# Optimization experiments

Hardware: AMD Instinct MI355X
Metric: run time of the kernel (lower is better)

Reference implementation:

```python
import jax, jax.numpy as jnp
import numpy as np

B, T, W, HP = 1, 64, 88, 48   # batch, frames, pitches, hidden_per_pitch
NU, NH, K = 24, 4, 25          # n_unit, n_heads, neighborhood window
HD = NU // NH                  # head dim = 6
HL = NU // 2                   # LSTM hidden per direction = 12


def _lstm_bidir(x, w_ih, w_hh, b_ih, b_hh):
    # x: [N, T, In]; w_ih: [2, 4*HL, In]; w_hh: [2, 4*HL, HL]; biases: [2, 4*HL]
    N = x.shape[0]
    def run(Wih, Whh, bih, bhh, reverse):
        def step(carry, xt):
            h, c = carry
            g = xt @ Wih.T + h @ Whh.T + bih + bhh
            i, f, gg, o = jnp.split(g, 4, axis=-1)  # torch gate order i,f,g,o
            c = jax.nn.sigmoid(f) * c + jax.nn.sigmoid(i) * jnp.tanh(gg)
            h = jax.nn.sigmoid(o) * jnp.tanh(c)
            return (h, c), h
        init = (jnp.zeros((N, HL), x.dtype), jnp.zeros((N, HL), x.dtype))
        _, ys = jax.lax.scan(step, init, jnp.swapaxes(x, 0, 1), reverse=reverse)
        return jnp.swapaxes(ys, 0, 1)
    return jnp.concatenate([run(w_ih[0], w_hh[0], b_ih[0], b_hh[0], False),
                            run(w_ih[1], w_hh[1], b_ih[1], b_hh[1], True)], axis=-1)


def _natten2d(x, qkv_w, qkv_b, rpb, proj_w, proj_b):
    # Neighborhood attention over 2D grid [B, Hh, Ww] with KxK window clamped at borders.
    Bn, Hh, Ww, C = x.shape
    qkv = (x @ qkv_w.T + qkv_b).reshape(Bn, Hh, Ww, 3, NH, HD)
    q = qkv[..., 0, :, :] * (HD ** -0.5)
    k = qkv[..., 1, :, :]
    v = qkv[..., 2, :, :]
    half = K // 2
    ar = jnp.arange(K)
    idx_i = jnp.clip(jnp.arange(Hh) - half, 0, Hh - K)[:, None] + ar  # [Hh,K]
    idx_j = jnp.clip(jnp.arange(Ww) - half, 0, Ww - K)[:, None] + ar  # [Ww,K]
    kg = k[:, idx_i][:, :, :, idx_j]  # [B,Hh,K,Ww,K,NH,HD]
    vg = v[:, idx_i][:, :, :, idx_j]
    ri = idx_i - jnp.arange(Hh)[:, None] + (K - 1)  # relative pos bias indices [Hh,K]
    rj = idx_j - jnp.arange(Ww)[:, None] + (K - 1)  # [Ww,K]
    bias = rpb[:, ri][:, :, :, rj]                  # [NH,Hh,K,Ww,K]
    logits = jnp.einsum('bijnd,biajcnd->bnijac', q, kg)
    logits = logits + jnp.transpose(bias, (0, 1, 3, 2, 4))[None]
    attn = jax.nn.softmax(logits.reshape(Bn, NH, Hh, Ww, K * K), axis=-1)
    attn = attn.reshape(Bn, NH, Hh, Ww, K, K)
    out = jnp.einsum('bnijac,biajcnd->bijnd', attn, vg).reshape(Bn, Hh, Ww, C)
    return out @ proj_w.T + proj_b


def _forward(features, condition, mask, emb, w_ih_l0, w_hh_l0, b_ih_l0, b_hh_l0,
             w_ih_l1, w_hh_l1, b_ih_l1, b_hh_l1, qkv_w, qkv_b, rpb, proj_w, proj_b,
             out_w, out_b):
    # concat: [B,T,88,HP] + [B,T,88,4] + [B,T,88,1] -> [B,T,88,HP+5]
    cat = jnp.concatenate([jnp.transpose(features, (0, 1, 3, 2)), emb[condition],
                           mask[..., None]], axis=-1)
    x = jnp.transpose(cat, (0, 2, 1, 3)).reshape(B * W, T, HP + 5)  # pitchwise LSTM
    x = _lstm_bidir(x, w_ih_l0, w_hh_l0, b_ih_l0, b_hh_l0)
    x = _lstm_bidir(x, w_ih_l1, w_hh_l1, b_ih_l1, b_hh_l1)
    x = jnp.transpose(x.reshape(B, W, T, NU), (0, 2, 1, 3))  # [B,T,88,NU]
    for _ in range(2):  # n_layers=2; Sequential(*[m]*2) => SHARED weights
        x = _natten2d(x, qkv_w, qkv_b, rpb, proj_w, proj_b)
    return x @ out_w.T + out_b  # [B,T,88,5]


def setup_inputs():
    ks = jax.random.split(jax.random.key(0), 24)
    def unif(k, shape, fan):
        s = 1.0 / np.sqrt(fan)
        return jax.random.uniform(k, shape, jnp.float32, -s, s)
    return {
        'features': jax.random.normal(ks[0], (B, T, HP, W), jnp.float32),
        'condition': jax.random.randint(ks[1], (B, T, W), 0, 5),
        'mask': jax.random.uniform(ks[2], (B, T, W), jnp.float32),
        'emb': jax.random.normal(ks[3], (5, 4), jnp.float32),
        'w_ih_l0': unif(ks[4], (2, 4 * HL, HP + 5), HL),
        'w_hh_l0': unif(ks[5], (2, 4 * HL, HL), HL),
        'b_ih_l0': unif(ks[6], (2, 4 * HL), HL),
        'b_hh_l0': unif(ks[7], (2, 4 * HL), HL),
        'w_ih_l1': unif(ks[8], (2, 4 * HL, 2 * HL), HL),
        'w_hh_l1': unif(ks[9], (2, 4 * HL, HL), HL),
        'b_ih_l1': unif(ks[10], (2, 4 * HL), HL),
        'b_hh_l1': unif(ks[11], (2, 4 * HL), HL),
        'qkv_w': unif(ks[12], (3 * NU, NU), NU),
        'qkv_b': unif(ks[13], (3 * NU,), NU),
        'rpb': jax.random.normal(ks[14], (NH, 2 * K - 1, 2 * K - 1), jnp.float32) * 0.02,
        'proj_w': unif(ks[15], (NU, NU), NU),
        'proj_b': unif(ks[16], (NU,), NU),
        'out_w': unif(ks[17], (5, NU), NU),
        'out_b': unif(ks[18], (5,), NU),
    }


def reference(features, condition, mask, emb, w_ih_l0, w_hh_l0, b_ih_l0, b_hh_l0,
              w_ih_l1, w_hh_l1, b_ih_l1, b_hh_l1, qkv_w, qkv_b, rpb, proj_w, proj_b,
              out_w, out_b):
    return _forward(features, condition, mask, emb, w_ih_l0, w_hh_l0, b_ih_l0, b_hh_l0,
                    w_ih_l1, w_hh_l1, b_ih_l1, b_hh_l1, qkv_w, qkv_b, rpb,
                    proj_w, proj_b, out_w, out_b)
```

## Files before the change

kernel.cpp:

```cpp
#include <hip/hip_runtime.h>
#include <hip/hip_bf16.h>

#define NPIX (64*88)
#define NSEQ 88
#define TT 64
#define F0 53
#define GATES 48

typedef __hip_bfloat16 bf16;

__device__ __forceinline__ float frcp(float x){ return __builtin_amdgcn_rcpf(x); }
__device__ __forceinline__ float blo(unsigned u){ return __uint_as_float(u<<16); }
__device__ __forceinline__ float bhi(unsigned u){ return __uint_as_float(u & 0xffff0000u); }

__device__ __forceinline__ void unpack6(uint4 r, float* f){
  f[0] = __uint_as_float(r.x << 16);
  f[1] = __uint_as_float(r.x & 0xffff0000u);
  f[2] = __uint_as_float(r.y << 16);
  f[3] = __uint_as_float(r.y & 0xffff0000u);
  f[4] = __uint_as_float(r.z << 16);
  f[5] = __uint_as_float(r.z & 0xffff0000u);
}

__global__ __launch_bounds__(1024) void k_core(
    const float* __restrict__ feat, const int* __restrict__ cond,
    const float* __restrict__ mask, const float* __restrict__ emb,
    const float* __restrict__ wih0, const float* __restrict__ whh0,
    const float* __restrict__ bih0, const float* __restrict__ bhh0,
    const float* __restrict__ wih1, const float* __restrict__ whh1,
    const float* __restrict__ bih1, const float* __restrict__ bhh1,
    const float* __restrict__ qkv_w, const float* __restrict__ qkv_b,
    float* __restrict__ q, bf16* __restrict__ kh, bf16* __restrict__ vh){
  int n = (blockIdx.x & 7)*11 + (blockIdx.x >> 3);
  int tid = threadIdx.x;
  int wave = tid >> 6; int lane = tid & 63;
  __shared__ float smem[14816];
  float* gbuf = smem;
  float* sx   = smem + 6144;
  float* sw0  = smem + 6144+3392;
  float* w1   = smem + 6144;
  float* sqkv = smem + 6144+2400;
  float* y0   = smem + 6144+4200;
  float* y1   = smem + 6144+5736;
  float* bsum = smem + 14624;

  for (int idx = tid; idx < 2*GATES*F0; idx += 1024) sw0[idx] = wih0[idx];
  for (int idx = tid; idx < TT*F0; idx += 1024){
    int t = idx / F0, f = idx - t*F0;
    float v;
    if (f < 48)      v = feat[(t*48 + f)*88 + n];
    else if (f < 52) v = emb[cond[t*88+n]*4 + (f-48)];
    else             v = mask[t*88+n];
    sx[idx] = v;
  }
  if (tid < 96)       bsum[tid] = bih0[tid] + bhh0[tid];
  else if (tid < 192) bsum[tid] = bih1[tid-96] + bhh1[tid-96];
  __syncthreads();

  #pragma unroll
  for (int r = 0; r < 6; ++r){
    int row = tid + r*1024;
    int d = row / 3072; int rem = row - d*3072;
    int t = rem / 48; int j = rem - t*48;
    const float* xr = sx + t*F0;
    const float* wr = sw0 + (d*GATES + j)*F0;
    float a0=0.f, a1=0.f, a2=0.f, a3=0.f;
    #pragma unroll
    for (int f=0; f<52; f+=4){
      a0 += xr[f  ]*wr[f  ];
      a1 += xr[f+1]*wr[f+1];
      a2 += xr[f+2]*wr[f+2];
      a3 += xr[f+3]*wr[f+3];
    }
    gbuf[(d*TT + t)*GATES + j] = bsum[d*GATES+j] + xr[52]*wr[52] + ((a0+a1)+(a2+a3));
  }
  __syncthreads();

  if (wave >= 2){
    for (int idx = tid-128; idx < 2*GATES*24; idx += 896){
      int row = idx / 24, f = idx - row*24;
      w1[row*25 + f] = wih1[idx];
    }
    for (int idx = tid-128; idx < 72*24; idx += 896){
      int row = idx / 24, f = idx - row*24;
      sqkv[row*25 + f] = qkv_w[idx];
    }
  } else {
    int d = wave;
    int j = (lane < GATES) ? lane : (lane - GATES);
    int u = j % 12; int grp = j / 12;
    float w[12];
    const float* wb = whh0 + (d*GATES + j)*12;
    #pragma unroll
    for (int m=0;m<12;++m) w[m] = wb[m];
    float negs  = (grp==2) ? -2.f : -1.f;
    float amul  = (grp==2) ?  2.f :  1.f;
    float aadd  = (grp==2) ? -1.f :  0.f;
    const float* gb = gbuf + d*TT*GATES + j;
    float hval = 0.f, cval = 0.f;
    int t0 = d ? (TT-1) : 0;
    float gnext = gb[t0*GATES];
    for (int s=0;s<TT;++s){
      int t = d ? (TT-1-s) : s;
      float gg = gnext;
      int tn = d ? max(TT-2-s,0) : min(s+1,TT-1);
      gnext = gb[tn*GATES];
      float h0=__shfl(hval,0), h1=__shfl(hval,1), h2=__shfl(hval,2);
      float h3=__shfl(hval,3), h4=__shfl(hval,4), h5=__shfl(hval,5);
      float h6=__shfl(hval,6), h7=__shfl(hval,7), h8=__shfl(hval,8);
      float h9=__shfl(hval,9), h10=__shfl(hval,10), h11=__shfl(hval,11);
      float a0 = gg + h0*w[0] + h4*w[4] + h8*w[8];
      float a1 = h1*w[1] + h5*w[5] + h9*w[9];
      float a2 = h2*w[2] + h6*w[6] + h10*w[10];
      float a3 = h3*w[3] + h7*w[7] + h11*w[11];
      float dot = (a0+a1)+(a2+a3);
      float act = amul*frcp(1.f + __expf(negs*dot)) + aadd;
      float ai = __shfl(act, u);
      float af = __shfl(act, u+12);
      float ag = __shfl(act, u+24);
      float ao = __shfl(act, u+36);
      float cn = af*cval + ai*ag;
      float th = 2.f*frcp(1.f + __expf(-2.f*cn)) - 1.f;
      hval = ao*th; cval = cn;
      if (lane < 12) y0[t*24 + d*12 + lane] = hval;
    }
  }
  __syncthreads();

  #pragma unroll
  for (int r = 0; r < 6; ++r){
    int row = tid + r*1024;
    int d = row / 3072; int rem = row - d*3072;
    int t = rem / 48; int j = rem - t*48;
    const float* xr = y0 + t*24;
    const float* wr = w1 + (d*GATES + j)*25;
    float a0=0.f, a1=0.f;
    #pragma unroll
    for (int c=0; c<24; c+=2){ a0 += xr[c]*wr[c]; a1 += xr[c+1]*wr[c+1]; }
    gbuf[(d*TT + t)*GATES + j] = bsum[96 + d*GATES+j] + a0 + a1;
  }
  __syncthreads();

  if (wave < 2){
    int d = wave;
    int j = (lane < GATES) ? lane : (lane - GATES);
    int u = j % 12; int grp = j / 12;
    float w[12];
    const float* wb = whh1 + (d*GATES + j)*12;
    #pragma unroll
    for (int m=0;m<12;++m) w[m] = wb[m];
    float negs  = (grp==2) ? -2.f : -1.f;
    float amul  = (grp==2) ?  2.f :  1.f;
    float aadd  = (grp==2) ? -1.f :  0.f;
    const float* gb = gbuf + d*TT*GATES + j;
    float hval = 0.f, cval = 0.f;
    int t0 = d ? (TT-1) : 0;
    float gnext = gb[t0*GATES];
    for (int s=0;s<TT;++s){
      int t = d ? (TT-1-s) : s;
      float gg = gnext;
      int tn = d ? max(TT-2-s,0) : min(s+1,TT-1);
      gnext = gb[tn*GATES];
      float h0=__shfl(hval,0), h1=__shfl(hval,1), h2=__shfl(hval,2);
      float h3=__shfl(hval,3), h4=__shfl(hval,4), h5=__shfl(hval,5);
      float h6=__shfl(hval,6), h7=__shfl(hval,7), h8=__shfl(hval,8);
      float h9=__shfl(hval,9), h10=__shfl(hval,10), h11=__shfl(hval,11);
      float a0 = gg + h0*w[0] + h4*w[4] + h8*w[8];
      float a1 = h1*w[1] + h5*w[5] + h9*w[9];
      float a2 = h2*w[2] + h6*w[6] + h10*w[10];
      float a3 = h3*w[3] + h7*w[7] + h11*w[11];
      float dot = (a0+a1)+(a2+a3);
      float act = amul*frcp(1.f + __expf(negs*dot)) + aadd;
      float ai = __shfl(act, u);
      float af = __shfl(act, u+12);
      float ag = __shfl(act, u+24);
      float ao = __shfl(act, u+36);
      float cn = af*cval + ai*ag;
      float th = 2.f*frcp(1.f + __expf(-2.f*cn)) - 1.f;
      hval = ao*th; cval = cn;
      if (lane < 12) y1[t*24 + d*12 + lane] = hval;
    }
  }
  __syncthreads();

  for (int idx = tid; idx < TT*72; idx += 1024){
    int gq = idx % 72; int t = idx / 72;
    int p = t*88 + n;
    const float* xr = y1 + t*24;
    const float* wr = sqkv + gq*25;
    float a0=0.f, a1=0.f;
    #pragma unroll
    for (int c=0; c<24; c+=2){ a0 += xr[c]*wr[c]; a1 += xr[c+1]*wr[c+1]; }
    float acc = qkv_b[gq] + a0 + a1;
    int s = gq/24, rem = gq - s*24;
    if (s==0) q[p*24+rem] = acc*0.4082482904638631f;
    else {
      int hh = rem/6, pos = rem - hh*6;
      bf16* dst = (s==1) ? kh : vh;
      dst[((size_t)hh*NPIX + p)*8 + pos] = __float2bfloat16(acc);
    }
  }
}

__global__ __launch_bounds__(256) void k_attn1(
    const float* __restrict__ q, const bf16* __restrict__ kh,
    const bf16* __restrict__ vh, const float* __restrict__ rpb,
    const float* __restrict__ pw, const float* __restrict__ pb,
    const float* __restrict__ qkv_w, const float* __restrict__ qkv_b,
    float* __restrict__ q2, bf16* __restrict__ kh2, bf16* __restrict__ vh2){
  int p = blockIdx.x; int tid = threadIdx.x;
  int h = tid >> 6; int lane = tid & 63;
  int i = p / 88, j = p - i*88;
  int si = min(max(i-12,0),39), sj = min(max(j-12,0),63);
  __shared__ float aorow[24];
  __shared__ float xrow[24];

  float qv[6];
  #pragma unroll
  for (int d=0; d<6; ++d) qv[d] = q[p*24 + h*6 + d];
  const uint4* kb = (const uint4*)(kh + (size_t)h*NPIX*8);
  const uint4* vb = (const uint4*)(vh + (size_t)h*NPIX*8);
  float lgv[10]; int roff[10];
  float lmax = -1e30f;
  #pragma unroll
  for (int it=0; it<10; ++it){
    int nb = lane + it*64;
    bool valid = nb < 625;
    int nbc = valid ? nb : 624;
    int a = nbc/25, cc = nbc - a*25;
    int gi = si + a, gj = sj + cc;
    int row = gi*88+gj;
    roff[it] = row;
    float kr[6];
    unpack6(kb[row], kr);
    float lg = qv[0]*kr[0]+qv[1]*kr[1]+qv[2]*kr[2]+qv[3]*kr[3]+qv[4]*kr[4]+qv[5]*kr[5];
    lg += rpb[(h*49 + (gi - i + 24))*49 + (gj - j + 24)];
    lg = valid ? lg : -1e30f;
    lgv[it] = lg;
    lmax = fmaxf(lmax, lg);
  }
  #pragma unroll
  for (int off=32; off; off>>=1) lmax = fmaxf(lmax, __shfl_xor(lmax, off));
  float lsum = 0.f;
  #pragma unroll
  for (int it=0; it<10; ++it){
    float pe = __expf(lgv[it]-lmax);
    lgv[it] = pe; lsum += pe;
  }
  #pragma unroll
  for (int off=32; off; off>>=1) lsum += __shfl_xor(lsum, off);
  float acc[6] = {0,0,0,0,0,0};
  #pragma unroll
  for (int it=0; it<10; ++it){
    float vr[6];
    unpack6(vb[roff[it]], vr);
    float pe = lgv[it];
    #pragma unroll
    for (int d=0; d<6; ++d) acc[d] += pe*vr[d];
  }
  #pragma unroll
  for (int d=0; d<6; ++d){
    #pragma unroll
    for (int off=32; off; off>>=1) acc[d] += __shfl_xor(acc[d], off);
  }
  if (lane == 0){
    float inv = frcp(lsum);
    #pragma unroll
    for (int d=0; d<6; ++d) aorow[h*6+d] = acc[d]*inv;
  }
  __syncthreads();

  if (tid < 24){
    float a2 = pb[tid];
    const float* wr = pw + tid*24;
    #pragma unroll
    for (int c=0;c<24;++c) a2 += aorow[c]*wr[c];
    xrow[tid] = a2;
  }
  __syncthreads();

  if (tid < 72){
    float a2 = qkv_b[tid];
    const float* wr = qkv_w + tid*24;
    #pragma unroll
    for (int c=0;c<24;++c) a2 += xrow[c]*wr[c];
    int s = tid/24, rem = tid - s*24;
    if (s==0) q2[p*24+rem] = a2*0.4082482904638631f;
    else {
      int hh = rem/6, pos = rem - hh*6;
      bf16* dst = (s==1) ? kh2 : vh2;
      dst[((size_t)hh*NPIX + p)*8 + pos] = __float2bfloat16(a2);
    }
  }
}

__global__ __launch_bounds__(512) void k_attn(
    const float* __restrict__ q, const bf16* __restrict__ kh,
    const bf16* __restrict__ vh, const float* __restrict__ rpb,
    float* __restrict__ ao){
  int b = blockIdx.x;
  int h = b / 704; int rem = b - h*704;
  int ti = rem / 44, tj = rem - ti*44;
  int i0 = ti*4, j0 = tj*2;
  int tid = threadIdx.x;
  int w = tid >> 6; int lane = tid & 63;
  int osi = min(max(i0-12,0),39);
  int osj = min(max(j0-12,0),63);

  __shared__ unsigned kt[728*5];
  __shared__ unsigned vt[728*5];
  const uint4* kg = (const uint4*)(kh + (size_t)h*NPIX*8);
  const uint4* vg = (const uint4*)(vh + (size_t)h*NPIX*8);
  for (int idx = tid; idx < 728; idx += 512){
    int a = idx / 26, cc = idx - a*26;
    int gi = min(osi + a, 63), gj = min(osj + cc, 87);
    int src = gi*88 + gj;
    uint4 kr = kg[src];
    uint4 vr = vg[src];
    int o = idx*5;
    kt[o] = kr.x; kt[o+1] = kr.y; kt[o+2] = kr.z;
    vt[o] = vr.x; vt[o+1] = vr.y; vt[o+2] = vr.z;
  }
  __syncthreads();

  int pi = i0 + (w>>1), pj = j0 + (w&1);
  int p = pi*88 + pj;
  int dsi = min(max(pi-12,0),39) - osi;
  int dsj = min(max(pj-12,0),63) - osj;
  int rbi = osi + dsi - pi + 24;
  int rbj = osj + dsj - pj + 24;

  float qv[6];
  #pragma unroll
  for (int d=0; d<6; ++d) qv[d] = q[p*24 + h*6 + d];

  float lgv[10]; int rof[10];
  float lmax = -1e30f;
  #pragma unroll
  for (int it=0; it<10; ++it){
    int nb = lane + it*64;
    bool valid = nb < 625;
    int nbc = valid ? nb : 624;
    int a = nbc/25, cc = nbc - a*25;
    int r5 = ((a+dsi)*26 + (cc+dsj))*5;
    rof[it] = r5;
    unsigned k0 = kt[r5], k1 = kt[r5+1], k2 = kt[r5+2];
    float lg = qv[0]*blo(k0)+qv[1]*bhi(k0)+qv[2]*blo(k1)
             + qv[3]*bhi(k1)+qv[4]*blo(k2)+qv[5]*bhi(k2);
    lg += rpb[(h*49 + (a + rbi))*49 + (cc + rbj)];
    lg = valid ? lg : -1e30f;
    lgv[it] = lg;
    lmax = fmaxf(lmax, lg);
  }
  #pragma unroll
  for (int off=32; off; off>>=1) lmax = fmaxf(lmax, __shfl_xor(lmax, off));
  float lsum = 0.f;
  #pragma unroll
  for (int it=0; it<10; ++it){
    float pe = __expf(lgv[it]-lmax);
    lgv[it] = pe; lsum += pe;
  }
  #pragma unroll
  for (int off=32; off; off>>=1) lsum += __shfl_xor(lsum, off);
  float acc[6] = {0,0,0,0,0,0};
  #pragma unroll
  for (int it=0; it<10; ++it){
    int r5 = rof[it];
    unsigned v0 = vt[r5], v1 = vt[r5+1], v2 = vt[r5+2];
    float pe = lgv[it];
    acc[0] += pe*blo(v0); acc[1] += pe*bhi(v0);
    acc[2] += pe*blo(v1); acc[3] += pe*bhi(v1);
    acc[4] += pe*blo(v2); acc[5] += pe*bhi(v2);
  }
  #pragma unroll
  for (int d=0; d<6; ++d){
    #pragma unroll
    for (int off=32; off; off>>=1) acc[d] += __shfl_xor(acc[d], off);
  }
  if (lane == 0){
    float inv = frcp(lsum);
    #pragma unroll
    for (int d=0; d<6; ++d) ao[p*24 + h*6 + d] = acc[d]*inv;
  }
}

__global__ __launch_bounds__(64) void k_proj_out(const float* __restrict__ ain,
    const float* __restrict__ pw, const float* __restrict__ pb,
    const float* __restrict__ ow, const float* __restrict__ ob,
    float* __restrict__ out){
  int p = blockIdx.x; int tid = threadIdx.x;
  __shared__ float arow[24];
  __shared__ float xrow[24];
  if (tid < 24) arow[tid] = ain[p*24+tid];
  __syncthreads();
  if (tid < 24){
    float a2 = pb[tid];
    const float* wr = pw + tid*24;
    #pragma unroll
    for (int c=0;c<24;++c) a2 += arow[c]*wr[c];
    xrow[tid] = a2;
  }
  __syncthreads();
  if (tid < 5){
    float a2 = ob[tid];
    const float* wr = ow + tid*24;
    #pragma unroll
    for (int c=0;c<24;++c) a2 += xrow[c]*wr[c];
    out[p*5+tid] = a2;
  }
}

extern "C" void kernel_launch(void* const* d_in, const int* in_sizes, int n_in,
                              void* d_out, int out_size, void* d_ws, size_t ws_size,
                              hipStream_t stream) {
  const float* feat    = (const float*)d_in[0];
  const int*   cond    = (const int*)  d_in[1];
  const float* mask    = (const float*)d_in[2];
  const float* emb     = (const float*)d_in[3];
  const float* w_ih_l0 = (const float*)d_in[4];
  const float* w_hh_l0 = (const float*)d_in[5];
  const float* b_ih_l0 = (const float*)d_in[6];
  const float* b_hh_l0 = (const float*)d_in[7];
  const float* w_ih_l1 = (const float*)d_in[8];
  const float* w_hh_l1 = (const float*)d_in[9];
  const float* b_ih_l1 = (const float*)d_in[10];
  const float* b_hh_l1 = (const float*)d_in[11];
  const float* qkv_w   = (const float*)d_in[12];
  const float* qkv_b   = (const float*)d_in[13];
  const float* rpb     = (const float*)d_in[14];
  const float* proj_w  = (const float*)d_in[15];
  const float* proj_b  = (const float*)d_in[16];
  const float* out_w   = (const float*)d_in[17];
  const float* out_b   = (const float*)d_in[18];
  float* out = (float*)d_out;

  float* ws  = (float*)d_ws;
  float* Q1  = ws;
  float* Q2  = Q1 + 135168;
  float* AO  = Q2 + 135168;
  bf16*  KH1 = (bf16*)(AO + 135168);
  bf16*  VH1 = KH1 + 180224;
  bf16*  KH2 = VH1 + 180224;
  bf16*  VH2 = KH2 + 180224;

  k_core<<<NSEQ, 1024, 0, stream>>>(
      feat, cond, mask, emb,
      w_ih_l0, w_hh_l0, b_ih_l0, b_hh_l0,
      w_ih_l1, w_hh_l1, b_ih_l1, b_hh_l1,
      qkv_w, qkv_b, Q1, KH1, VH1);

  k_attn1<<<NPIX, 256, 0, stream>>>(
      Q1, KH1, VH1, rpb, proj_w, proj_b, qkv_w, qkv_b,
      Q2, KH2, VH2);

  k_attn<<<4*16*44, 512, 0, stream>>>(Q2, KH2, VH2, rpb, AO);

  k_proj_out<<<NPIX, 64, 0, stream>>>(AO, proj_w, proj_b, out_w, out_b, out);
}
```

Before: 204.6 us.

## Fuse projections into tiled attention kernels via per-head atomic accumulation

Replaces the per-pixel first attention kernel with the shared-memory tiled variant. Both attention passes now fold the following linear layers into per-head partial products: qkv·proj for the first pass and out·proj for the second. Each head atomically adds its contribution into zeroed fp32 Q2/K/V and output buffers, so the separate proj_out kernel and the AO buffer go away. The zero-fill is moved into the LSTM kernel. The cost is float atomics, redundant recomputation of the combined weight matrices in every block, and fp32 K/V for the second pass, which doubles its tile loads.

```diff
diff --git a/kernel.cpp b/kernel.cpp
--- a/kernel.cpp
+++ b/kernel.cpp
@@ -13,14 +13,7 @@
 __device__ __forceinline__ float blo(unsigned u){ return __uint_as_float(u<<16); }
 __device__ __forceinline__ float bhi(unsigned u){ return __uint_as_float(u & 0xffff0000u); }
 
-__device__ __forceinline__ void unpack6(uint4 r, float* f){
-  f[0] = __uint_as_float(r.x << 16);
-  f[1] = __uint_as_float(r.x & 0xffff0000u);
-  f[2] = __uint_as_float(r.y << 16);
-  f[3] = __uint_as_float(r.y & 0xffff0000u);
-  f[4] = __uint_as_float(r.z << 16);
-  f[5] = __uint_as_float(r.z & 0xffff0000u);
-}
+#define QSCALE 0.4082482904638631f
 
 __global__ __launch_bounds__(1024) void k_core(
     const float* __restrict__ feat, const int* __restrict__ cond,
@@ -30,10 +23,15 @@
     const float* __restrict__ wih1, const float* __restrict__ whh1,
     const float* __restrict__ bih1, const float* __restrict__ bhh1,
     const float* __restrict__ qkv_w, const float* __restrict__ qkv_b,
-    float* __restrict__ q, bf16* __restrict__ kh, bf16* __restrict__ vh){
+    float* __restrict__ q, bf16* __restrict__ kh, bf16* __restrict__ vh,
+    float* __restrict__ zq, float* __restrict__ outz){
   int n = (blockIdx.x & 7)*11 + (blockIdx.x >> 3);
   int tid = threadIdx.x;
   int wave = tid >> 6; int lane = tid & 63;
+
+  for (int idx = blockIdx.x*1024 + tid; idx < 495616; idx += 90112) zq[idx] = 0.f;
+  for (int idx = blockIdx.x*1024 + tid; idx < NPIX*5; idx += 90112) outz[idx] = 0.f;
+
   __shared__ float smem[14816];
   float* gbuf = smem;
   float* sx   = smem + 6144;
@@ -193,7 +191,7 @@
     for (int c=0; c<24; c+=2){ a0 += xr[c]*wr[c]; a1 += xr[c+1]*wr[c+1]; }
     float acc = qkv_b[gq] + a0 + a1;
     int s = gq/24, rem = gq - s*24;
-    if (s==0) q[p*24+rem] = acc*0.4082482904638631f;
+    if (s==0) q[p*24+rem] = acc*QSCALE;
     else {
       int hh = rem/6, pos = rem - hh*6;
       bf16* dst = (s==1) ? kh : vh;
@@ -202,102 +200,12 @@
   }
 }
 
-__global__ __launch_bounds__(256) void k_attn1(
+__global__ __launch_bounds__(512) void k_attn1t(
     const float* __restrict__ q, const bf16* __restrict__ kh,
     const bf16* __restrict__ vh, const float* __restrict__ rpb,
     const float* __restrict__ pw, const float* __restrict__ pb,
     const float* __restrict__ qkv_w, const float* __restrict__ qkv_b,
-    float* __restrict__ q2, bf16* __restrict__ kh2, bf16* __restrict__ vh2){
-  int p = blockIdx.x; int tid = threadIdx.x;
-  int h = tid >> 6; int lane = tid & 63;
-  int i = p / 88, j = p - i*88;
-  int si = min(max(i-12,0),39), sj = min(max(j-12,0),63);
-  __shared__ float aorow[24];
-  __shared__ float xrow[24];
-
-  float qv[6];
-  #pragma unroll
-  for (int d=0; d<6; ++d) qv[d] = q[p*24 + h*6 + d];
-  const uint4* kb = (const uint4*)(kh + (size_t)h*NPIX*8);
-  const uint4* vb = (const uint4*)(vh + (size_t)h*NPIX*8);
-  float lgv[10]; int roff[10];
-  float lmax = -1e30f;
-  #pragma unroll
-  for (int it=0; it<10; ++it){
-    int nb = lane + it*64;
-    bool valid = nb < 625;
-    int nbc = valid ? nb : 624;
-    int a = nbc/25, cc = nbc - a*25;
-    int gi = si + a, gj = sj + cc;
-    int row = gi*88+gj;
-    roff[it] = row;
-    float kr[6];
-    unpack6(kb[row], kr);
-    float lg = qv[0]*kr[0]+qv[1]*kr[1]+qv[2]*kr[2]+qv[3]*kr[3]+qv[4]*kr[4]+qv[5]*kr[5];
-    lg += rpb[(h*49 + (gi - i + 24))*49 + (gj - j + 24)];
-    lg = valid ? lg : -1e30f;
-    lgv[it] = lg;
-    lmax = fmaxf(lmax, lg);
-  }
-  #pragma unroll
-  for (int off=32; off; off>>=1) lmax = fmaxf(lmax, __shfl_xor(lmax, off));
-  float lsum = 0.f;
-  #pragma unroll
-  for (int it=0; it<10; ++it){
-    float pe = __expf(lgv[it]-lmax);
-    lgv[it] = pe; lsum += pe;
-  }
-  #pragma unroll
-  for (int off=32; off; off>>=1) lsum += __shfl_xor(lsum, off);
-  float acc[6] = {0,0,0,0,0,0};
-  #pragma unroll
-  for (int it=0; it<10; ++it){
-    float vr[6];
-    unpack6(vb[roff[it]], vr);
-    float pe = lgv[it];
-    #pragma unroll
-    for (int d=0; d<6; ++d) acc[d] += pe*vr[d];
-  }
-  #pragma unroll
-  for (int d=0; d<6; ++d){
-    #pragma unroll
-    for (int off=32; off; off>>=1) acc[d] += __shfl_xor(acc[d], off);
-  }
-  if (lane == 0){
-    float inv = frcp(lsum);
-    #pragma unroll
-    for (int d=0; d<6; ++d) aorow[h*6+d] = acc[d]*inv;
-  }
-  __syncthreads();
-
-  if (tid < 24){
-    float a2 = pb[tid];
-    const float* wr = pw + tid*24;
-    #pragma unroll
-    for (int c=0;c<24;++c) a2 += aorow[c]*wr[c];
-    xrow[tid] = a2;
-  }
-  __syncthreads();
-
-  if (tid < 72){
-    float a2 = qkv_b[tid];
-    const float* wr = qkv_w + tid*24;
-    #pragma unroll
-    for (int c=0;c<24;++c) a2 += xrow[c]*wr[c];
-    int s = tid/24, rem = tid - s*24;
-    if (s==0) q2[p*24+rem] = a2*0.4082482904638631f;
-    else {
-      int hh = rem/6, pos = rem - hh*6;
-      bf16* dst = (s==1) ? kh2 : vh2;
-      dst[((size_t)hh*NPIX + p)*8 + pos] = __float2bfloat16(a2);
-    }
-  }
-}
-
-__global__ __launch_bounds__(512) void k_attn(
-    const float* __restrict__ q, const bf16* __restrict__ kh,
-    const bf16* __restrict__ vh, const float* __restrict__ rpb,
-    float* __restrict__ ao){
+    float* __restrict__ q2, float* __restrict__ kh2f, float* __restrict__ vh2f){
   int b = blockIdx.x;
   int h = b / 704; int rem = b - h*704;
   int ti = rem / 44, tj = rem - ti*44;
@@ -309,6 +217,13 @@
 
   __shared__ unsigned kt[728*5];
   __shared__ unsigned vt[728*5];
+  __shared__ float spw[24*24];
+  __shared__ float sqw[72*24];
+  __shared__ float spb[24];
+  __shared__ float M[72*25];
+  __shared__ float bq[72];
+  __shared__ float aorow[8][6];
+
   const uint4* kg = (const uint4*)(kh + (size_t)h*NPIX*8);
   const uint4* vg = (const uint4*)(vh + (size_t)h*NPIX*8);
   for (int idx = tid; idx < 728; idx += 512){
@@ -321,6 +236,9 @@
     kt[o] = kr.x; kt[o+1] = kr.y; kt[o+2] = kr.z;
     vt[o] = vr.x; vt[o+1] = vr.y; vt[o+2] = vr.z;
   }
+  for (int idx = tid; idx < 576; idx += 512) spw[idx] = pw[idx];
+  for (int idx = tid; idx < 1728; idx += 512) sqw[idx] = qkv_w[idx];
+  if (tid < 24) spb[tid] = pb[tid];
   __syncthreads();
 
   int pi = i0 + (w>>1), pj = j0 + (w&1);
@@ -380,33 +298,169 @@
   if (lane == 0){
     float inv = frcp(lsum);
     #pragma unroll
-    for (int d=0; d<6; ++d) ao[p*24 + h*6 + d] = acc[d]*inv;
+    for (int d=0; d<6; ++d) aorow[w][d] = acc[d]*inv;
+  }
+  __syncthreads();
+
+  for (int idx = tid; idx < 1728; idx += 512){
+    int g = idx / 24, c = idx - g*24;
+    const float* qr = sqw + g*24;
+    float a2 = 0.f;
+    #pragma unroll
+    for (int k=0;k<24;++k) a2 += qr[k]*spw[k*24+c];
+    M[g*25+c] = a2;
+  }
+  if (tid < 72){
+    const float* qr = sqw + tid*24;
+    float a2 = qkv_b[tid];
+    #pragma unroll
+    for (int k=0;k<24;++k) a2 += qr[k]*spb[k];
+    bq[tid] = a2;
+  }
+  __syncthreads();
+
+  for (int idx = tid; idx < 576; idx += 512){
+    int pp = idx / 72, g = idx - pp*72;
+    int pg = (i0 + (pp>>1))*88 + (j0 + (pp&1));
+    const float* ar = aorow[pp];
+    const float* mr = M + g*25 + h*6;
+    float val = ar[0]*mr[0]+ar[1]*mr[1]+ar[2]*mr[2]
+              + ar[3]*mr[3]+ar[4]*mr[4]+ar[5]*mr[5];
+    if (h == 0) val += bq[g];
+    int s = g/24, rm = g - s*24;
+    if (s==0) atomicAdd(&q2[pg*24+rm], val*QSCALE);
+    else {
+      int hh = rm/6, pos = rm - hh*6;
+      float* dst = (s==1) ? kh2f : vh2f;
+      atomicAdd(&dst[((size_t)hh*NPIX + pg)*8 + pos], val);
+    }
   }
 }
 
-__global__ __launch_bounds__(64) void k_proj_out(const float* __restrict__ ain,
+__global__ __launch_bounds__(512) void k_attn2t(
+    const float* __restrict__ q, const float* __restrict__ khf,
+    const float* __restrict__ vhf, const float* __restrict__ rpb,
     const float* __restrict__ pw, const float* __restrict__ pb,
     const float* __restrict__ ow, const float* __restrict__ ob,
     float* __restrict__ out){
-  int p = blockIdx.x; int tid = threadIdx.x;
-  __shared__ float arow[24];
-  __shared__ float xrow[24];
-  if (tid < 24) arow[tid] = ain[p*24+tid];
-  __syncthreads();
-  if (tid < 24){
-    float a2 = pb[tid];
-    const float* wr = pw + tid*24;
-    #pragma unroll
-    for (int c=0;c<24;++c) a2 += arow[c]*wr[c];
-    xrow[tid] = a2;
-  }
-  __syncthreads();
+  int b = blockIdx.x;
+  int h = b / 704; int rem = b - h*704;
+  int ti = rem / 44, tj = rem - ti*44;
+  int i0 = ti*4, j0 = tj*2;
+  int tid = threadIdx.x;
+  int w = tid >> 6; int lane = tid & 63;
+  int osi = min(max(i0-12,0),39);
+  int osj = min(max(j0-12,0),63);
+
+  __shared__ float kt[728*7];
+  __shared__ float vt[728*7];
+  __shared__ float spw[24*24];
+  __shared__ float sow[5*24];
+  __shared__ float E[5*25];
+  __shared__ float eb[5];
+  __shared__ float aorow[8][6];
+
+  const float4* kg = (const float4*)(khf + (size_t)h*NPIX*8);
+  const float4* vg = (const float4*)(vhf + (size_t)h*NPIX*8);
+  for (int idx = tid; idx < 728; idx += 512){
+    int a = idx / 26, cc = idx - a*26;
+    int gi = min(osi + a, 63), gj = min(osj + cc, 87);
+    int src = gi*88 + gj;
+    float4 k0 = kg[src*2], k1 = kg[src*2+1];
+    float4 v0 = vg[src*2], v1 = vg[src*2+1];
+    int o = idx*7;
+    kt[o]=k0.x; kt[o+1]=k0.y; kt[o+2]=k0.z; kt[o+3]=k0.w; kt[o+4]=k1.x; kt[o+5]=k1.y;
+    vt[o]=v0.x; vt[o+1]=v0.y; vt[o+2]=v0.z; vt[o+3]=v0.w; vt[o+4]=v1.x; vt[o+5]=v1.y;
+  }
+  for (int idx = tid; idx < 576; idx += 512) spw[idx] = pw[idx];
+  if (tid < 120) sow[tid] = ow[tid];
+  __syncthreads();
+
+  int pi = i0 + (w>>1), pj = j0 + (w&1);
+  int p = pi*88 + pj;
+  int dsi = min(max(pi-12,0),39) - osi;
+  int dsj = min(max(pj-12,0),63) - osj;
+  int rbi = osi + dsi - pi + 24;
+  int rbj = osj + dsj - pj + 24;
+
+  float qv[6];
+  #pragma unroll
+  for (int d=0; d<6; ++d) qv[d] = q[p*24 + h*6 + d];
+
+  float lgv[10]; int rof[10];
+  float lmax = -1e30f;
+  #pragma unroll
+  for (int it=0; it<10; ++it){
+    int nb = lane + it*64;
+    bool valid = nb < 625;
+    int nbc = valid ? nb : 624;
+    int a = nbc/25, cc = nbc - a*25;
+    int r7 = ((a+dsi)*26 + (cc+dsj))*7;
+    rof[it] = r7;
+    float lg = qv[0]*kt[r7]+qv[1]*kt[r7+1]+qv[2]*kt[r7+2]
+             + qv[3]*kt[r7+3]+qv[4]*kt[r7+4]+qv[5]*kt[r7+5];
+    lg += rpb[(h*49 + (a + rbi))*49 + (cc + rbj)];
+    lg = valid ? lg : -1e30f;
+    lgv[it] = lg;
+    lmax = fmaxf(lmax, lg);
+  }
+  #pragma unroll
+  for (int off=32; off; off>>=1) lmax = fmaxf(lmax, __shfl_xor(lmax, off));
+  float lsum = 0.f;
+  #pragma unroll
+  for (int it=0; it<10; ++it){
+    float pe = __expf(lgv[it]-lmax);
+    lgv[it] = pe; lsum += pe;
+  }
+  #pragma unroll
+  for (int off=32; off; off>>=1) lsum += __shfl_xor(lsum, off);
+  float acc[6] = {0,0,0,0,0,0};
+  #pragma unroll
+  for (int it=0; it<10; ++it){
+    int r7 = rof[it];
+    float pe = lgv[it];
+    acc[0] += pe*vt[r7];   acc[1] += pe*vt[r7+1];
+    acc[2] += pe*vt[r7+2]; acc[3] += pe*vt[r7+3];
+    acc[4] += pe*vt[r7+4]; acc[5] += pe*vt[r7+5];
+  }
+  #pragma unroll
+  for (int d=0; d<6; ++d){
+    #pragma unroll
+    for (int off=32; off; off>>=1) acc[d] += __shfl_xor(acc[d], off);
+  }
+  if (lane == 0){
+    float inv = frcp(lsum);
+    #pragma unroll
+    for (int d=0; d<6; ++d) aorow[w][d] = acc[d]*inv;
+  }
+  __syncthreads();
+
+  if (tid < 120){
+    int o = tid / 24, c = tid - o*24;
+    const float* orr = sow + o*24;
+    float a2 = 0.f;
+    #pragma unroll
+    for (int k=0;k<24;++k) a2 += orr[k]*spw[k*24+c];
+    E[o*25+c] = a2;
+  }
   if (tid < 5){
+    const float* orr = sow + tid*24;
     float a2 = ob[tid];
-    const float* wr = ow + tid*24;
-    #pragma unroll
-    for (int c=0;c<24;++c) a2 += xrow[c]*wr[c];
-    out[p*5+tid] = a2;
+    #pragma unroll
+    for (int k=0;k<24;++k) a2 += orr[k]*pb[k];
+    eb[tid] = a2;
+  }
+  __syncthreads();
+
+  if (tid < 40){
+    int pp = tid / 5, o = tid - pp*5;
+    int pg = (i0 + (pp>>1))*88 + (j0 + (pp&1));
+    const float* ar = aorow[pp];
+    const float* er = E + o*25 + h*6;
+    float val = ar[0]*er[0]+ar[1]*er[1]+ar[2]*er[2]
+              + ar[3]*er[3]+ar[4]*er[4]+ar[5]*er[5];
+    if (h == 0) val += eb[o];
+    atomicAdd(&out[pg*5+o], val);
   }
 }
 
@@ -434,26 +488,24 @@
   const float* out_b   = (const float*)d_in[18];
   float* out = (float*)d_out;
 
-  float* ws  = (float*)d_ws;
-  float* Q1  = ws;
-  float* Q2  = Q1 + 135168;
-  float* AO  = Q2 + 135168;
-  bf16*  KH1 = (bf16*)(AO + 135168);
-  bf16*  VH1 = KH1 + 180224;
-  bf16*  KH2 = VH1 + 180224;
-  bf16*  VH2 = KH2 + 180224;
+  float* ws   = (float*)d_ws;
+  float* Q1   = ws;
+  float* Q2   = Q1 + 135168;
+  float* KH2f = Q2 + 135168;
+  float* VH2f = KH2f + 180224;
+  bf16*  KH1  = (bf16*)(VH2f + 180224);
+  bf16*  VH1  = KH1 + 180224;
 
   k_core<<<NSEQ, 1024, 0, stream>>>(
       feat, cond, mask, emb,
       w_ih_l0, w_hh_l0, b_ih_l0, b_hh_l0,
       w_ih_l1, w_hh_l1, b_ih_l1, b_hh_l1,
-      qkv_w, qkv_b, Q1, KH1, VH1);
-
-  k_attn1<<<NPIX, 256, 0, stream>>>(
+      qkv_w, qkv_b, Q1, KH1, VH1, Q2, out);
+
+  k_attn1t<<<4*16*44, 512, 0, stream>>>(
       Q1, KH1, VH1, rpb, proj_w, proj_b, qkv_w, qkv_b,
-      Q2, KH2, VH2);
-
-  k_attn<<<4*16*44, 512, 0, stream>>>(Q2, KH2, VH2, rpb, AO);
-
-  k_proj_out<<<NPIX, 64, 0, stream>>>(AO, proj_w, proj_b, out_w, out_b, out);
+      Q2, KH2f, VH2f);
+
+  k_attn2t<<<4*16*44, 512, 0, stream>>>(
+      Q2, KH2f, VH2f, rpb, proj_w, proj_b, out_w, out_b, out);
 }
```

New measurement: 228.7 us. 11.8% more time.

## Fuse projection and output heads into attention kernel via per-head atomics

Applied to the files above, without the earlier changes.

Removes the separate per-pixel projection/output kernel by folding proj_w and out_w into a combined 5x24 matrix inside the second attention kernel. Each head block adds its partial output contribution into the final output with atomicAdd, and the bias is added once by head 0. The output buffer is zeroed at the start of the first kernel, and the intermediate AO buffer goes away. This saves one launch and a global round-trip. In exchange, every attention block now computes the fused matrix redundantly and adds atomic traffic, and the float summation order becomes nondeterministic.

```diff
diff --git a/kernel.cpp b/kernel.cpp
--- a/kernel.cpp
+++ b/kernel.cpp
@@ -12,6 +12,8 @@
 __device__ __forceinline__ float frcp(float x){ return __builtin_amdgcn_rcpf(x); }
 __device__ __forceinline__ float blo(unsigned u){ return __uint_as_float(u<<16); }
 __device__ __forceinline__ float bhi(unsigned u){ return __uint_as_float(u & 0xffff0000u); }
+
+#define QSCALE 0.4082482904638631f
 
 __device__ __forceinline__ void unpack6(uint4 r, float* f){
   f[0] = __uint_as_float(r.x << 16);
@@ -30,10 +32,14 @@
     const float* __restrict__ wih1, const float* __restrict__ whh1,
     const float* __restrict__ bih1, const float* __restrict__ bhh1,
     const float* __restrict__ qkv_w, const float* __restrict__ qkv_b,
-    float* __restrict__ q, bf16* __restrict__ kh, bf16* __restrict__ vh){
+    float* __restrict__ q, bf16* __restrict__ kh, bf16* __restrict__ vh,
+    float* __restrict__ outz){
   int n = (blockIdx.x & 7)*11 + (blockIdx.x >> 3);
   int tid = threadIdx.x;
   int wave = tid >> 6; int lane = tid & 63;
+
+  for (int idx = blockIdx.x*1024 + tid; idx < NPIX*5; idx += 90112) outz[idx] = 0.f;
+
   __shared__ float smem[14816];
   float* gbuf = smem;
   float* sx   = smem + 6144;
@@ -193,7 +199,7 @@
     for (int c=0; c<24; c+=2){ a0 += xr[c]*wr[c]; a1 += xr[c+1]*wr[c+1]; }
     float acc = qkv_b[gq] + a0 + a1;
     int s = gq/24, rem = gq - s*24;
-    if (s==0) q[p*24+rem] = acc*0.4082482904638631f;
+    if (s==0) q[p*24+rem] = acc*QSCALE;
     else {
       int hh = rem/6, pos = rem - hh*6;
       bf16* dst = (s==1) ? kh : vh;
@@ -285,7 +291,7 @@
     #pragma unroll
     for (int c=0;c<24;++c) a2 += xrow[c]*wr[c];
     int s = tid/24, rem = tid - s*24;
-    if (s==0) q2[p*24+rem] = a2*0.4082482904638631f;
+    if (s==0) q2[p*24+rem] = a2*QSCALE;
     else {
       int hh = rem/6, pos = rem - hh*6;
       bf16* dst = (s==1) ? kh2 : vh2;
@@ -294,10 +300,12 @@
   }
 }
 
-__global__ __launch_bounds__(512) void k_attn(
+__global__ __launch_bounds__(512) void k_attn2t(
     const float* __restrict__ q, const bf16* __restrict__ kh,
     const bf16* __restrict__ vh, const float* __restrict__ rpb,
-    float* __restrict__ ao){
+    const float* __restrict__ pw, const float* __restrict__ pb,
+    const float* __restrict__ ow, const float* __restrict__ ob,
+    float* __restrict__ out){
   int b = blockIdx.x;
   int h = b / 704; int rem = b - h*704;
   int ti = rem / 44, tj = rem - ti*44;
@@ -309,6 +317,12 @@
 
   __shared__ unsigned kt[728*5];
   __shared__ unsigned vt[728*5];
+  __shared__ float spw[24*24];
+  __shared__ float sow[5*24];
+  __shared__ float E[5*25];
+  __shared__ float eb[5];
+  __shared__ float aorow[8][6];
+
   const uint4* kg = (const uint4*)(kh + (size_t)h*NPIX*8);
   const uint4* vg = (const uint4*)(vh + (size_t)h*NPIX*8);
   for (int idx = tid; idx < 728; idx += 512){
@@ -321,6 +335,8 @@
     kt[o] = kr.x; kt[o+1] = kr.y; kt[o+2] = kr.z;
     vt[o] = vr.x; vt[o+1] = vr.y; vt[o+2] = vr.z;
   }
+  for (int idx = tid; idx < 576; idx += 512) spw[idx] = pw[idx];
+  if (tid < 120) sow[tid] = ow[tid];
   __syncthreads();
 
   int pi = i0 + (w>>1), pj = j0 + (w&1);
@@ -380,33 +396,36 @@
   if (lane == 0){
     float inv = frcp(lsum);
     #pragma unroll
-    for (int d=0; d<6; ++d) ao[p*24 + h*6 + d] = acc[d]*inv;
-  }
-}
-
-__global__ __launch_bounds__(64) void k_proj_out(const float* __restrict__ ain,
-    const float* __restrict__ pw, const float* __restrict__ pb,
-    const float* __restrict__ ow, const float* __restrict__ ob,
-    float* __restrict__ out){
-  int p = blockIdx.x; int tid = threadIdx.x;
-  __shared__ float arow[24];
-  __shared__ float xrow[24];
-  if (tid < 24) arow[tid] = ain[p*24+tid];
-  __syncthreads();
-  if (tid < 24){
-    float a2 = pb[tid];
-    const float* wr = pw + tid*24;
-    #pragma unroll
-    for (int c=0;c<24;++c) a2 += arow[c]*wr[c];
-    xrow[tid] = a2;
-  }
-  __syncthreads();
-  if (tid < 5){
-    float a2 = ob[tid];
-    const float* wr = ow + tid*24;
-    #pragma unroll
-    for (int c=0;c<24;++c) a2 += xrow[c]*wr[c];
-    out[p*5+tid] = a2;
+    for (int d=0; d<6; ++d) aorow[w][d] = acc[d]*inv;
+  }
+
+  if (tid < 120){
+    int o = tid / 24, c = tid - o*24;
+    const float* orr = sow + o*24;
+    float a2 = 0.f;
+    #pragma unroll
+    for (int k=0;k<24;++k) a2 += orr[k]*spw[k*24+c];
+    E[o*25+c] = a2;
+  }
+  if (tid >= 128 && tid < 133){
+    int o = tid - 128;
+    const float* orr = sow + o*24;
+    float a2 = ob[o];
+    #pragma unroll
+    for (int k=0;k<24;++k) a2 += orr[k]*pb[k];
+    eb[o] = a2;
+  }
+  __syncthreads();
+
+  if (tid < 40){
+    int pp = tid / 5, o = tid - pp*5;
+    int pg = (i0 + (pp>>1))*88 + (j0 + (pp&1));
+    const float* ar = aorow[pp];
+    const float* er = E + o*25 + h*6;
+    float val = ar[0]*er[0]+ar[1]*er[1]+ar[2]*er[2]
+              + ar[3]*er[3]+ar[4]*er[4]+ar[5]*er[5];
+    if (h == 0) val += eb[o];
+    atomicAdd(&out[pg*5+o], val);
   }
 }
 
@@ -437,8 +456,7 @@
   float* ws  = (float*)d_ws;
   float* Q1  = ws;
   float* Q2  = Q1 + 135168;
-  float* AO  = Q2 + 135168;
-  bf16*  KH1 = (bf16*)(AO + 135168);
+  bf16*  KH1 = (bf16*)(Q2 + 135168);
   bf16*  VH1 = KH1 + 180224;
   bf16*  KH2 = VH1 + 180224;
   bf16*  VH2 = KH2 + 180224;
@@ -447,13 +465,12 @@
       feat, cond, mask, emb,
       w_ih_l0, w_hh_l0, b_ih_l0, b_hh_l0,
       w_ih_l1, w_hh_l1, b_ih_l1, b_hh_l1,
-      qkv_w, qkv_b, Q1, KH1, VH1);
+      qkv_w, qkv_b, Q1, KH1, VH1, out);
 
   k_attn1<<<NPIX, 256, 0, stream>>>(
       Q1, KH1, VH1, rpb, proj_w, proj_b, qkv_w, qkv_b,
       Q2, KH2, VH2);
 
-  k_attn<<<4*16*44, 512, 0, stream>>>(Q2, KH2, VH2, rpb, AO);
-
-  k_proj_out<<<NPIX, 64, 0, stream>>>(AO, proj_w, proj_b, out_w, out_b, out);
+  k_attn2t<<<4*16*44, 512, 0, stream>>>(
+      Q2, KH2, VH2, rpb, proj_w, proj_b, out_w, out_b, out);
 }
```

New measurement: 206.1 us. No clear change (+0.7%).
